# Kernel optimization log

Measured on AMD Instinct MI355X. Metric: run time of the kernel, lower is better.

Reference implementation:

```python
import jax, jax.numpy as jnp
import numpy as np

B, S, D, E, F, A = 4096, 256, 128, 64, 4, 32
CD = D * F              # combined_dim = 512
LEVEL_N = [16, 4, 1]    # aggregators per tree level (fan_in**i for i=2,1,0)
TOTAL = E + sum(LEVEL_N)  # 85 embeddings stacked

def _init(key, shape, fan_in):
    return jax.random.normal(key, shape, jnp.float32) / np.sqrt(fan_in)

def setup_inputs() -> dict:
    key = jax.random.key(0)
    ks = iter(jax.random.split(key, 64))
    inp = {"state": jax.random.normal(next(ks), (B, S), jnp.float32)}
    # 64 encoder FNNs: S -> D -> D -> D, stacked along leading node axis
    inp["enc_w1"] = _init(next(ks), (E, S, D), S); inp["enc_b1"] = jnp.zeros((E, D), jnp.float32)
    inp["enc_wh"] = _init(next(ks), (E, D, D), D); inp["enc_bh"] = jnp.zeros((E, D), jnp.float32)
    inp["enc_wo"] = _init(next(ks), (E, D, D), D); inp["enc_bo"] = jnp.zeros((E, D), jnp.float32)
    # aggregator FNNs per level: CD -> CD -> CD -> D
    for li, n in enumerate(LEVEL_N):
        inp[f"agg{li}_w1"] = _init(next(ks), (n, CD, CD), CD); inp[f"agg{li}_b1"] = jnp.zeros((n, CD), jnp.float32)
        inp[f"agg{li}_wh"] = _init(next(ks), (n, CD, CD), CD); inp[f"agg{li}_bh"] = jnp.zeros((n, CD), jnp.float32)
        inp[f"agg{li}_wo"] = _init(next(ks), (n, CD, D), CD);  inp[f"agg{li}_bo"] = jnp.zeros((n, D), jnp.float32)
    # head FNN: D -> D -> D -> A
    inp["head_w1"] = _init(next(ks), (D, D), D); inp["head_b1"] = jnp.zeros((D,), jnp.float32)
    inp["head_wh"] = _init(next(ks), (D, D), D); inp["head_bh"] = jnp.zeros((D,), jnp.float32)
    inp["head_wo"] = _init(next(ks), (D, A), D); inp["head_bo"] = jnp.zeros((A,), jnp.float32)
    return inp

def _fnn(x, w1, b1, wh, bh, wo, bo):
    # x: [N,B,I] batched over N independent same-shaped FNNs (grouped GEMM form)
    h = jax.nn.relu(jnp.einsum('nbi,nih->nbh', x, w1) + b1[:, None])
    h = jax.nn.relu(jnp.einsum('nbh,nhk->nbk', h, wh) + bh[:, None])
    return jnp.einsum('nbh,nho->nbo', h, wo) + bo[:, None]

def _forward(state, enc_w1, enc_b1, enc_wh, enc_bh, enc_wo, enc_bo,
             agg0_w1, agg0_b1, agg0_wh, agg0_bh, agg0_wo, agg0_bo,
             agg1_w1, agg1_b1, agg1_wh, agg1_bh, agg1_wo, agg1_bo,
             agg2_w1, agg2_b1, agg2_wh, agg2_bh, agg2_wo, agg2_bo,
             head_w1, head_b1, head_wh, head_bh, head_wo, head_bo):
    # encoders: state [B,S] shared across all E encoders
    h = jax.nn.relu(jnp.einsum('bs,nsh->nbh', state, enc_w1) + enc_b1[:, None])
    h = jax.nn.relu(jnp.einsum('nbh,nhk->nbk', h, enc_wh) + enc_bh[:, None])
    prev = jnp.einsum('nbh,nho->nbo', h, enc_wo) + enc_bo[:, None]   # [E,B,D]
    all_embeds = [prev]
    levels = [(agg0_w1, agg0_b1, agg0_wh, agg0_bh, agg0_wo, agg0_bo),
              (agg1_w1, agg1_b1, agg1_wh, agg1_bh, agg1_wo, agg1_bo),
              (agg2_w1, agg2_b1, agg2_wh, agg2_bh, agg2_wo, agg2_bo)]
    for (w1, b1, wh, bh, wo, bo) in levels:
        n = prev.shape[0] // F
        # concat fan-in sibling embeddings along feature dim: [n,B,F*D]
        x = prev.reshape(n, F, B, D).transpose(0, 2, 1, 3).reshape(n, B, F * D)
        prev = _fnn(x, w1, b1, wh, bh, wo, bo)                        # [n,B,D]
        all_embeds.append(prev)
    root = prev[0]                                                    # [B,D]
    hh = jax.nn.relu(root @ head_w1 + head_b1)
    hh = jax.nn.relu(hh @ head_wh + head_bh)
    action = jnp.tanh(hh @ head_wo + head_bo)                         # noise_std=0.0, action_tanh=True
    embeds = jnp.transpose(jnp.concatenate(all_embeds, axis=0), (1, 0, 2))  # [B,85,D]
    return embeds, action

def reference(state, enc_w1, enc_b1, enc_wh, enc_bh, enc_wo, enc_bo,
              agg0_w1, agg0_b1, agg0_wh, agg0_bh, agg0_wo, agg0_bo,
              agg1_w1, agg1_b1, agg1_wh, agg1_bh, agg1_wo, agg1_bo,
              agg2_w1, agg2_b1, agg2_wh, agg2_bh, agg2_wo, agg2_bo,
              head_w1, head_b1, head_wh, head_bh, head_wo, head_bo):
    return _forward(state, enc_w1, enc_b1, enc_wh, enc_bh, enc_wo, enc_bo,
                    agg0_w1, agg0_b1, agg0_wh, agg0_bh, agg0_wo, agg0_bo,
                    agg1_w1, agg1_b1, agg1_wh, agg1_bh, agg1_wo, agg1_bo,
                    agg2_w1, agg2_b1, agg2_wh, agg2_bh, agg2_wo, agg2_bo,
                    head_w1, head_b1, head_wh, head_bh, head_wo, head_bo)
```

## Files before the change

### kernel.cpp

```cpp
#include <hip/hip_runtime.h>
#include <math.h>

typedef unsigned short u16;
typedef __bf16 bf16x8 __attribute__((ext_vector_type(8)));
typedef float  f32x4  __attribute__((ext_vector_type(4)));

__device__ __forceinline__ u16 f2bf(float f) {
    unsigned int u = __float_as_uint(f);
    u = (u + 0x7FFFu + ((u >> 16) & 1u)) >> 16;
    return (u16)u;
}

__device__ __forceinline__ void gload16(const u16* g, u16* l) {
    __builtin_amdgcn_global_load_lds(
        (const __attribute__((address_space(1))) void*)g,
        (__attribute__((address_space(3))) void*)l, 16, 0, 0);
}

struct TJob { const float* src; u16* dst; int K, N, tpg, gbase, mode; };
struct TTab { TJob j[16]; };

__global__ void transpose_multi(TTab tab, int njobs) {
    __shared__ u16 tile[32][33];
    int bid = blockIdx.x;
    int ji = 0;
#pragma unroll 1
    for (int t = 1; t < njobs; ++t)
        if (bid >= tab.j[t].gbase) ji = t;
    TJob jb = tab.j[ji];
    int t = bid - jb.gbase;
    if (jb.mode == 1) {
        long off = (long)t * 1024 + threadIdx.x * 4;
        float4 x = *(const float4*)(jb.src + off);
        ushort4 o;
        o.x = f2bf(x.x); o.y = f2bf(x.y); o.z = f2bf(x.z); o.w = f2bf(x.w);
        *(ushort4*)(jb.dst + off) = o;
        return;
    }
    int g = t / jb.tpg, r = t % jb.tpg;
    int nt = jb.N >> 5;
    int k0 = (r / nt) * 32, n0 = (r % nt) * 32;
    const float* s = jb.src + (long)g * jb.K * jb.N;
    u16* d = jb.dst + (long)g * jb.K * jb.N;
    int tx = threadIdx.x & 31, ty = threadIdx.x >> 5;
#pragma unroll
    for (int rr = ty; rr < 32; rr += 8)
        tile[rr][tx] = f2bf(s[(long)(k0 + rr) * jb.N + n0 + tx]);
    __syncthreads();
#pragma unroll
    for (int rr = ty; rr < 32; rr += 8)
        d[(long)(n0 + rr) * jb.K + k0 + tx] = tile[tx][rr];
}

__global__ __launch_bounds__(256, 2)
void fnn_chain128(const u16* __restrict__ X, long sXg, int ldx, int K1,
                  const u16* __restrict__ W1t, const float* __restrict__ b1,
                  const u16* __restrict__ Wht, const float* __restrict__ bh,
                  const u16* __restrict__ Wot, const float* __restrict__ bo,
                  int Do, int act3,
                  float* __restrict__ Cf, long sCfg, int ldcf,
                  u16* __restrict__ Cb, long sCbg, int ldcb)
{
    __shared__ __align__(16) u16 As[2][128 * 32];
    __shared__ __align__(16) u16 Bs[2][128 * 32];
    __shared__ __align__(16) u16 h[128 * 152];

    const int g   = blockIdx.y;
    const int m0  = blockIdx.x * 128;
    const int tid = threadIdx.x;
    const int lane = tid & 63, wv = tid >> 6;
    const int wm = wv & 1, wn = wv >> 1;
    const int lr = lane & 15, lq = lane >> 4;
    const int row0 = tid >> 2, c8 = (tid & 3) * 8;

    const u16* a_src = X + (long)g * sXg + (long)(m0 + row0) * ldx + c8;
    const u16* w1r   = W1t + (long)g * 128 * K1 + (long)row0 * K1 + c8;
    const u16* whr   = Wht + (long)g * 128 * 128 + (long)row0 * 128 + c8;

    const f32x4 z4 = {0.f, 0.f, 0.f, 0.f};
    f32x4 acc[4][4];
#pragma unroll
    for (int i = 0; i < 4; ++i)
#pragma unroll
        for (int j = 0; j < 4; ++j) acc[i][j] = z4;

    const int KT1 = K1 >> 5;
    auto stage1 = [&](int buf, int k0) {
        gload16(a_src + k0,                  &As[buf][row0 * 32 + c8]);
        gload16(a_src + (long)64 * ldx + k0, &As[buf][(row0 + 64) * 32 + c8]);
        gload16(w1r + k0,                    &Bs[buf][row0 * 32 + c8]);
        gload16(w1r + (long)64 * K1 + k0,    &Bs[buf][(row0 + 64) * 32 + c8]);
    };
    stage1(0, 0);
    __syncthreads();
    for (int kt = 0; kt < KT1; ++kt) {
        int cur = kt & 1;
        if (kt + 1 < KT1) stage1(cur ^ 1, (kt + 1) * 32);
        bf16x8 af[4], bw[4];
#pragma unroll
        for (int i = 0; i < 4; ++i)
            af[i] = *(const bf16x8*)&As[cur][(wm * 64 + i * 16 + lr) * 32 + lq * 8];
#pragma unroll
        for (int j = 0; j < 4; ++j)
            bw[j] = *(const bf16x8*)&Bs[cur][(wn * 64 + j * 16 + lr) * 32 + lq * 8];
#pragma unroll
        for (int i = 0; i < 4; ++i)
#pragma unroll
            for (int j = 0; j < 4; ++j)
                acc[i][j] = __builtin_amdgcn_mfma_f32_16x16x32_bf16(
                    af[i], bw[j], acc[i][j], 0, 0, 0);
        __syncthreads();
    }
    {
        const float* bg = b1 + (long)g * 128;
#pragma unroll
        for (int j = 0; j < 4; ++j) {
            int n = wn * 64 + j * 16 + lr;
            float bb = bg[n];
#pragma unroll
            for (int i = 0; i < 4; ++i) {
                int mb = wm * 64 + i * 16 + lq * 4;
#pragma unroll
                for (int r = 0; r < 4; ++r)
                    h[(mb + r) * 152 + n] = f2bf(fmaxf(acc[i][j][r] + bb, 0.f));
            }
        }
    }

#pragma unroll
    for (int i = 0; i < 4; ++i)
#pragma unroll
        for (int j = 0; j < 4; ++j) acc[i][j] = z4;
    auto stage2 = [&](int buf, int k0) {
        gload16(whr + k0,                  &Bs[buf][row0 * 32 + c8]);
        gload16(whr + (long)64 * 128 + k0, &Bs[buf][(row0 + 64) * 32 + c8]);
    };
    stage2(0, 0);
    __syncthreads();
    for (int kt = 0; kt < 4; ++kt) {
        int cur = kt & 1;
        if (kt + 1 < 4) stage2(cur ^ 1, (kt + 1) * 32);
        bf16x8 af[4], bw[4];
#pragma unroll
        for (int i = 0; i < 4; ++i)
            af[i] = *(const bf16x8*)&h[(wm * 64 + i * 16 + lr) * 152 + kt * 32 + lq * 8];
#pragma unroll
        for (int j = 0; j < 4; ++j)
            bw[j] = *(const bf16x8*)&Bs[cur][(wn * 64 + j * 16 + lr) * 32 + lq * 8];
#pragma unroll
        for (int i = 0; i < 4; ++i)
#pragma unroll
            for (int j = 0; j < 4; ++j)
                acc[i][j] = __builtin_amdgcn_mfma_f32_16x16x32_bf16(
                    af[i], bw[j], acc[i][j], 0, 0, 0);
        __syncthreads();
    }
    {
        const float* bg = bh + (long)g * 128;
#pragma unroll
        for (int j = 0; j < 4; ++j) {
            int n = wn * 64 + j * 16 + lr;
            float bb = bg[n];
#pragma unroll
            for (int i = 0; i < 4; ++i) {
                int mb = wm * 64 + i * 16 + lq * 4;
#pragma unroll
                for (int r = 0; r < 4; ++r)
                    h[(mb + r) * 152 + n] = f2bf(fmaxf(acc[i][j][r] + bb, 0.f));
            }
        }
    }

#pragma unroll
    for (int i = 0; i < 4; ++i)
#pragma unroll
        for (int j = 0; j < 4; ++j) acc[i][j] = z4;
    const int nr0 = (row0 < Do) ? row0 : Do - 1;
    const int nr1 = (row0 + 64 < Do) ? row0 + 64 : Do - 1;
    const u16* wor0 = Wot + (long)g * Do * 128 + (long)nr0 * 128 + c8;
    const u16* wor1 = Wot + (long)g * Do * 128 + (long)nr1 * 128 + c8;
    auto stage3 = [&](int buf, int k0) {
        gload16(wor0 + k0, &Bs[buf][row0 * 32 + c8]);
        gload16(wor1 + k0, &Bs[buf][(row0 + 64) * 32 + c8]);
    };
    stage3(0, 0);
    __syncthreads();
    for (int kt = 0; kt < 4; ++kt) {
        int cur = kt & 1;
        if (kt + 1 < 4) stage3(cur ^ 1, (kt + 1) * 32);
        bf16x8 af[4], bw[4];
#pragma unroll
        for (int i = 0; i < 4; ++i)
            af[i] = *(const bf16x8*)&h[(wm * 64 + i * 16 + lr) * 152 + kt * 32 + lq * 8];
#pragma unroll
        for (int j = 0; j < 4; ++j)
            bw[j] = *(const bf16x8*)&Bs[cur][(wn * 64 + j * 16 + lr) * 32 + lq * 8];
#pragma unroll
        for (int i = 0; i < 4; ++i)
#pragma unroll
            for (int j = 0; j < 4; ++j)
                acc[i][j] = __builtin_amdgcn_mfma_f32_16x16x32_bf16(
                    af[i], bw[j], acc[i][j], 0, 0, 0);
        __syncthreads();
    }
    {
        const float* bg = bo + (long)g * Do;
#pragma unroll
        for (int j = 0; j < 4; ++j) {
            int n = wn * 64 + j * 16 + lr;
            if (n >= Do) continue;
            float bb = bg[n];
#pragma unroll
            for (int i = 0; i < 4; ++i) {
                int mb = wm * 64 + i * 16 + lq * 4;
#pragma unroll
                for (int r = 0; r < 4; ++r) {
                    float v = acc[i][j][r] + bb;
                    if (act3 == 2) v = tanhf(v);
                    long mrow = m0 + mb + r;
                    Cf[(long)g * sCfg + mrow * ldcf + n] = v;
                    if (Cb) Cb[(long)g * sCbg + mrow * ldcb + n] = f2bf(v);
                }
            }
        }
    }
}

__global__ __launch_bounds__(512, 2)
void fnn_chain512(const u16* __restrict__ X, long sXg, int ldx,
                  const u16* __restrict__ W1t, const float* __restrict__ b1,
                  const u16* __restrict__ Wht, const float* __restrict__ bh,
                  const u16* __restrict__ Wot, const float* __restrict__ bo,
                  float* __restrict__ Cf, long sCfg, int ldcf,
                  u16* __restrict__ Cb, long sCbg, int ldcb)
{
    __shared__ __align__(16) u16 As[2][64 * 32];
    __shared__ __align__(16) u16 Bs[2][512 * 32];
    __shared__ __align__(16) u16 h[64 * 536];

    const int g   = blockIdx.y;
    const int m0  = blockIdx.x * 64;
    const int tid = threadIdx.x;
    const int lane = tid & 63, wv = tid >> 6;
    const int lr = lane & 15, lq = lane >> 4;
    const int row0 = tid >> 2, c8 = (tid & 3) * 8;

    const u16* a_src = X + (long)g * sXg + (long)(m0 + row0) * ldx + c8;
    const u16* w1r = W1t + (long)g * 512 * 512 + (long)row0 * 512 + c8;
    const u16* whr = Wht + (long)g * 512 * 512 + (long)row0 * 512 + c8;
    const u16* wor = Wot + (long)g * 128 * 512 + (long)row0 * 512 + c8;

    const f32x4 z4 = {0.f, 0.f, 0.f, 0.f};
    f32x4 acc[4][4];
#pragma unroll
    for (int i = 0; i < 4; ++i)
#pragma unroll
        for (int j = 0; j < 4; ++j) acc[i][j] = z4;

    auto stage1 = [&](int buf, int k0) {
        if (tid < 256) gload16(a_src + k0, &As[buf][row0 * 32 + c8]);
#pragma unroll
        for (int r = 0; r < 4; ++r)
            gload16(w1r + (long)(128 * r) * 512 + k0,
                    &Bs[buf][(row0 + 128 * r) * 32 + c8]);
    };
    stage1(0, 0);
    __syncthreads();
    for (int kt = 0; kt < 16; ++kt) {
        int cur = kt & 1;
        if (kt + 1 < 16) stage1(cur ^ 1, (kt + 1) * 32);
        bf16x8 af[4], bw[4];
#pragma unroll
        for (int i = 0; i < 4; ++i)
            af[i] = *(const bf16x8*)&As[cur][(i * 16 + lr) * 32 + lq * 8];
#pragma unroll
        for (int j = 0; j < 4; ++j)
            bw[j] = *(const bf16x8*)&Bs[cur][(wv * 64 + j * 16 + lr) * 32 + lq * 8];
#pragma unroll
        for (int i = 0; i < 4; ++i)
#pragma unroll
            for (int j = 0; j < 4; ++j)
                acc[i][j] = __builtin_amdgcn_mfma_f32_16x16x32_bf16(
                    af[i], bw[j], acc[i][j], 0, 0, 0);
        __syncthreads();
    }
    {
        const float* bg = b1 + (long)g * 512;
#pragma unroll
        for (int j = 0; j < 4; ++j) {
            int n = wv * 64 + j * 16 + lr;
            float bb = bg[n];
#pragma unroll
            for (int i = 0; i < 4; ++i) {
                int mb = i * 16 + lq * 4;
#pragma unroll
                for (int r = 0; r < 4; ++r)
                    h[(mb + r) * 536 + n] = f2bf(fmaxf(acc[i][j][r] + bb, 0.f));
            }
        }
    }

#pragma unroll
    for (int i = 0; i < 4; ++i)
#pragma unroll
        for (int j = 0; j < 4; ++j) acc[i][j] = z4;
    auto stage2 = [&](int buf, int k0) {
#pragma unroll
        for (int r = 0; r < 4; ++r)
            gload16(whr + (long)(128 * r) * 512 + k0,
                    &Bs[buf][(row0 + 128 * r) * 32 + c8]);
    };
    stage2(0, 0);
    __syncthreads();
    for (int kt = 0; kt < 16; ++kt) {
        int cur = kt & 1;
        if (kt + 1 < 16) stage2(cur ^ 1, (kt + 1) * 32);
        bf16x8 af[4], bw[4];
#pragma unroll
        for (int i = 0; i < 4; ++i)
            af[i] = *(const bf16x8*)&h[(i * 16 + lr) * 536 + kt * 32 + lq * 8];
#pragma unroll
        for (int j = 0; j < 4; ++j)
            bw[j] = *(const bf16x8*)&Bs[cur][(wv * 64 + j * 16 + lr) * 32 + lq * 8];
#pragma unroll
        for (int i = 0; i < 4; ++i)
#pragma unroll
            for (int j = 0; j < 4; ++j)
                acc[i][j] = __builtin_amdgcn_mfma_f32_16x16x32_bf16(
                    af[i], bw[j], acc[i][j], 0, 0, 0);
        __syncthreads();
    }
    {
        const float* bg = bh + (long)g * 512;
#pragma unroll
        for (int j = 0; j < 4; ++j) {
            int n = wv * 64 + j * 16 + lr;
            float bb = bg[n];
#pragma unroll
            for (int i = 0; i < 4; ++i) {
                int mb = i * 16 + lq * 4;
#pragma unroll
                for (int r = 0; r < 4; ++r)
                    h[(mb + r) * 536 + n] = f2bf(fmaxf(acc[i][j][r] + bb, 0.f));
            }
        }
    }

    const int wm3 = wv & 1, wn3 = wv >> 1;
    f32x4 a2[2][2];
#pragma unroll
    for (int i = 0; i < 2; ++i)
#pragma unroll
        for (int j = 0; j < 2; ++j) a2[i][j] = z4;
    auto stage3 = [&](int buf, int k0) {
        gload16(wor + k0, &Bs[buf][row0 * 32 + c8]);
    };
    stage3(0, 0);
    __syncthreads();
    for (int kt = 0; kt < 16; ++kt) {
        int cur = kt & 1;
        if (kt + 1 < 16) stage3(cur ^ 1, (kt + 1) * 32);
        bf16x8 af2[2], bw2[2];
#pragma unroll
        for (int i = 0; i < 2; ++i)
            af2[i] = *(const bf16x8*)&h[(wm3 * 32 + i * 16 + lr) * 536 + kt * 32 + lq * 8];
#pragma unroll
        for (int j = 0; j < 2; ++j)
            bw2[j] = *(const bf16x8*)&Bs[cur][(wn3 * 32 + j * 16 + lr) * 32 + lq * 8];
#pragma unroll
        for (int i = 0; i < 2; ++i)
#pragma unroll
            for (int j = 0; j < 2; ++j)
                a2[i][j] = __builtin_amdgcn_mfma_f32_16x16x32_bf16(
                    af2[i], bw2[j], a2[i][j], 0, 0, 0);
        __syncthreads();
    }
    {
        const float* bg = bo + (long)g * 128;
#pragma unroll
        for (int j = 0; j < 2; ++j) {
            int n = wn3 * 32 + j * 16 + lr;
            float bb = bg[n];
#pragma unroll
            for (int i = 0; i < 2; ++i) {
                int mb = wm3 * 32 + i * 16 + lq * 4;
#pragma unroll
                for (int r = 0; r < 4; ++r) {
                    float v = a2[i][j][r] + bb;
                    long mrow = m0 + mb + r;
                    Cf[(long)g * sCfg + mrow * ldcf + n] = v;
                    if (Cb) Cb[(long)g * sCbg + mrow * ldcb + n] = f2bf(v);
                }
            }
        }
    }
}

extern "C" void kernel_launch(void* const* d_in, const int* in_sizes, int n_in,
                              void* d_out, int out_size, void* d_ws, size_t ws_size,
                              hipStream_t stream) {
    const int B = 4096, S = 256, D = 128, NA = 32, CD = 512;

    const float* state   = (const float*)d_in[0];
    const float* enc_w1  = (const float*)d_in[1];
    const float* enc_b1  = (const float*)d_in[2];
    const float* enc_wh  = (const float*)d_in[3];
    const float* enc_bh  = (const float*)d_in[4];
    const float* enc_wo  = (const float*)d_in[5];
    const float* enc_bo  = (const float*)d_in[6];
    const float *agg_w1[3], *agg_b1[3], *agg_wh[3], *agg_bh[3], *agg_wo[3], *agg_bo[3];
    for (int l = 0; l < 3; ++l) {
        agg_w1[l] = (const float*)d_in[7 + 6 * l + 0];
        agg_b1[l] = (const float*)d_in[7 + 6 * l + 1];
        agg_wh[l] = (const float*)d_in[7 + 6 * l + 2];
        agg_bh[l] = (const float*)d_in[7 + 6 * l + 3];
        agg_wo[l] = (const float*)d_in[7 + 6 * l + 4];
        agg_bo[l] = (const float*)d_in[7 + 6 * l + 5];
    }
    const float* head_w1 = (const float*)d_in[25];
    const float* head_b1 = (const float*)d_in[26];
    const float* head_wh = (const float*)d_in[27];
    const float* head_bh = (const float*)d_in[28];
    const float* head_wo = (const float*)d_in[29];
    const float* head_bo = (const float*)d_in[30];

    float* out    = (float*)d_out;
    float* action = out + (long)B * 85 * D;

    char* wsp = (char*)d_ws;
    auto carve = [&](long elems) {
        u16* p = (u16*)wsp;
        wsp += ((elems * 2 + 255) / 256) * 256;
        return p;
    };
    u16* enc_w1t = carve(64L * 128 * 256);
    u16* enc_wht = carve(64L * 128 * 128);
    u16* enc_wot = carve(64L * 128 * 128);
    u16 *agg_w1t[3], *agg_wht[3], *agg_wot[3];
    const int LN[3] = {16, 4, 1};
    for (int l = 0; l < 3; ++l) {
        agg_w1t[l] = carve((long)LN[l] * 512 * 512);
        agg_wht[l] = carve((long)LN[l] * 512 * 512);
        agg_wot[l] = carve((long)LN[l] * 128 * 512);
    }
    u16* head_w1t = carve(128L * 128);
    u16* head_wht = carve(128L * 128);
    u16* head_wot = carve(32L * 128);
    u16* stateB = carve((long)B * S);
    u16* bufA   = carve(33554432L);
    u16* bufB   = carve(33554432L);

    TTab tab = {};
    int nj = 0, base = 0;
    auto addT = [&](const float* s, u16* d, int G, int K, int N) {
        int tpg = (K / 32) * (N / 32);
        tab.j[nj] = {s, d, K, N, tpg, base, 0};
        base += G * tpg; ++nj;
    };
    auto addC = [&](const float* s, u16* d, long elems) {
        tab.j[nj] = {s, d, 0, 0, 0, base, 1};
        base += (int)(elems / 1024); ++nj;
    };
    addT(enc_w1, enc_w1t, 64, 256, 128);
    addT(enc_wh, enc_wht, 64, 128, 128);
    addT(enc_wo, enc_wot, 64, 128, 128);
    for (int l = 0; l < 3; ++l) {
        addT(agg_w1[l], agg_w1t[l], LN[l], 512, 512);
        addT(agg_wh[l], agg_wht[l], LN[l], 512, 512);
        addT(agg_wo[l], agg_wot[l], LN[l], 512, 128);
    }
    addT(head_w1, head_w1t, 1, 128, 128);
    addT(head_wh, head_wht, 1, 128, 128);
    addT(head_wo, head_wot, 1, 128, 32);
    addC(state, stateB, (long)B * S);
    transpose_multi<<<base, 256, 0, stream>>>(tab, nj);

    const int LD = 85 * D;

    fnn_chain128<<<dim3(32, 64), 256, 0, stream>>>(
        stateB, 0, S, 256,
        enc_w1t, enc_b1, enc_wht, enc_bh, enc_wot, enc_bo, 128, 0,
        out, D, LD, bufA, D, 64 * D);

    fnn_chain512<<<dim3(64, 16), 512, 0, stream>>>(
        bufA, 512, 64 * D,
        agg_w1t[0], agg_b1[0], agg_wht[0], agg_bh[0], agg_wot[0], agg_bo[0],
        out + 64L * D, D, LD, bufB, D, 16 * D);

    fnn_chain512<<<dim3(64, 4), 512, 0, stream>>>(
        bufB, 512, 16 * D,
        agg_w1t[1], agg_b1[1], agg_wht[1], agg_bh[1], agg_wot[1], agg_bo[1],
        out + 80L * D, D, LD, bufA, D, 4 * D);

    fnn_chain512<<<dim3(64, 1), 512, 0, stream>>>(
        bufA, 0, 4 * D,
        agg_w1t[2], agg_b1[2], agg_wht[2], agg_bh[2], agg_wot[2], agg_bo[2],
        out + 84L * D, D, LD, bufB, 0, D);

    fnn_chain128<<<dim3(32, 1), 256, 0, stream>>>(
        bufB, 0, D, 128,
        head_w1t, head_b1, head_wht, head_bh, head_wot, head_bo, 32, 2,
        action, 0, NA, nullptr, 0, 0);
}
```

Baseline: 702.0 us.

## Halve row tiles, XOR-swizzle hidden LDS buffer, and split aggregator N into passes

Both fused FNN chain kernels now process half as many batch rows per block: 64 for the encoder/head kernel and 32 for the aggregator kernel. The aggregator kernel drops from 512 to 256 threads and computes its 512-wide hidden layers in two 256-column passes. The hidden activation buffer replaces padding with an XOR swizzle, which shrinks LDS and avoids bank conflicts. The aim is more blocks and higher occupancy, especially for the small last tree levels, at the cost of loading each weight tile twice as often per batch row.

```diff
diff --git a/kernel.cpp b/kernel.cpp
--- a/kernel.cpp
+++ b/kernel.cpp
@@ -15,6 +15,10 @@
     __builtin_amdgcn_global_load_lds(
         (const __attribute__((address_space(1))) void*)g,
         (__attribute__((address_space(3))) void*)l, 16, 0, 0);
+}
+
+__device__ __forceinline__ int hswz(int row, int col, int ld) {
+    return (row * ld + col) ^ ((row & 7) << 3);
 }
 
 struct TJob { const float* src; u16* dst; int K, N, tpg, gbase, mode; };
@@ -52,7 +56,7 @@
         d[(long)(n0 + rr) * jb.K + k0 + tx] = tile[tx][rr];
 }
 
-__global__ __launch_bounds__(256, 2)
+__global__ __launch_bounds__(256, 4)
 void fnn_chain128(const u16* __restrict__ X, long sXg, int ldx, int K1,
                   const u16* __restrict__ W1t, const float* __restrict__ b1,
                   const u16* __restrict__ Wht, const float* __restrict__ bh,
@@ -61,50 +65,49 @@
                   float* __restrict__ Cf, long sCfg, int ldcf,
                   u16* __restrict__ Cb, long sCbg, int ldcb)
 {
-    __shared__ __align__(16) u16 As[2][128 * 32];
+    __shared__ __align__(16) u16 As[2][64 * 32];
     __shared__ __align__(16) u16 Bs[2][128 * 32];
-    __shared__ __align__(16) u16 h[128 * 152];
+    __shared__ __align__(16) u16 h[64 * 128];
 
     const int g   = blockIdx.y;
-    const int m0  = blockIdx.x * 128;
+    const int m0  = blockIdx.x * 64;
     const int tid = threadIdx.x;
     const int lane = tid & 63, wv = tid >> 6;
     const int wm = wv & 1, wn = wv >> 1;
     const int lr = lane & 15, lq = lane >> 4;
-    const int row0 = tid >> 2, c8 = (tid & 3) * 8;
-
-    const u16* a_src = X + (long)g * sXg + (long)(m0 + row0) * ldx + c8;
-    const u16* w1r   = W1t + (long)g * 128 * K1 + (long)row0 * K1 + c8;
-    const u16* whr   = Wht + (long)g * 128 * 128 + (long)row0 * 128 + c8;
+    const int arow = tid >> 2, akc = (tid & 3) * 8;
+
+    const u16* a_src = X + (long)g * sXg + (long)(m0 + arow) * ldx + akc;
+    const u16* w1r   = W1t + (long)g * 128 * K1 + (long)arow * K1 + akc;
+    const u16* whr   = Wht + (long)g * 128 * 128 + (long)arow * 128 + akc;
 
     const f32x4 z4 = {0.f, 0.f, 0.f, 0.f};
-    f32x4 acc[4][4];
-#pragma unroll
-    for (int i = 0; i < 4; ++i)
+    f32x4 acc[2][4];
+#pragma unroll
+    for (int i = 0; i < 2; ++i)
 #pragma unroll
         for (int j = 0; j < 4; ++j) acc[i][j] = z4;
 
     const int KT1 = K1 >> 5;
     auto stage1 = [&](int buf, int k0) {
-        gload16(a_src + k0,                  &As[buf][row0 * 32 + c8]);
-        gload16(a_src + (long)64 * ldx + k0, &As[buf][(row0 + 64) * 32 + c8]);
-        gload16(w1r + k0,                    &Bs[buf][row0 * 32 + c8]);
-        gload16(w1r + (long)64 * K1 + k0,    &Bs[buf][(row0 + 64) * 32 + c8]);
+        gload16(a_src + k0, &As[buf][arow * 32 + akc]);
+        gload16(w1r + k0,                   &Bs[buf][arow * 32 + akc]);
+        gload16(w1r + (long)64 * K1 + k0,   &Bs[buf][(arow + 64) * 32 + akc]);
     };
     stage1(0, 0);
     __syncthreads();
     for (int kt = 0; kt < KT1; ++kt) {
         int cur = kt & 1;
         if (kt + 1 < KT1) stage1(cur ^ 1, (kt + 1) * 32);
-        bf16x8 af[4], bw[4];
-#pragma unroll
-        for (int i = 0; i < 4; ++i)
-            af[i] = *(const bf16x8*)&As[cur][(wm * 64 + i * 16 + lr) * 32 + lq * 8];
+        bf16x8 af[2], bw[4];
+#pragma unroll
+        for (int i = 0; i < 2; ++i)
+            af[i] = *(const bf16x8*)&As[cur][(wm * 32 + i * 16 + lr) * 32 + lq * 8];
 #pragma unroll
         for (int j = 0; j < 4; ++j)
             bw[j] = *(const bf16x8*)&Bs[cur][(wn * 64 + j * 16 + lr) * 32 + lq * 8];
 #pragma unroll
-        for (int i = 0; i < 4; ++i)
+        for (int i = 0; i < 2; ++i)
 #pragma unroll
             for (int j = 0; j < 4; ++j)
                 acc[i][j] = __builtin_amdgcn_mfma_f32_16x16x32_bf16(
@@ -118,37 +121,39 @@
             int n = wn * 64 + j * 16 + lr;
             float bb = bg[n];
 #pragma unroll
-            for (int i = 0; i < 4; ++i) {
-                int mb = wm * 64 + i * 16 + lq * 4;
+            for (int i = 0; i < 2; ++i) {
+                int mb = wm * 32 + i * 16 + lq * 4;
 #pragma unroll
                 for (int r = 0; r < 4; ++r)
-                    h[(mb + r) * 152 + n] = f2bf(fmaxf(acc[i][j][r] + bb, 0.f));
-            }
-        }
-    }
-
-#pragma unroll
-    for (int i = 0; i < 4; ++i)
+                    h[hswz(mb + r, n, 128)] = f2bf(fmaxf(acc[i][j][r] + bb, 0.f));
+            }
+        }
+    }
+
+#pragma unroll
+    for (int i = 0; i < 2; ++i)
 #pragma unroll
         for (int j = 0; j < 4; ++j) acc[i][j] = z4;
     auto stage2 = [&](int buf, int k0) {
-        gload16(whr + k0,                  &Bs[buf][row0 * 32 + c8]);
-        gload16(whr + (long)64 * 128 + k0, &Bs[buf][(row0 + 64) * 32 + c8]);
+        gload16(whr + k0,                  &Bs[buf][arow * 32 + akc]);
+        gload16(whr + (long)64 * 128 + k0, &Bs[buf][(arow + 64) * 32 + akc]);
     };
     stage2(0, 0);
     __syncthreads();
     for (int kt = 0; kt < 4; ++kt) {
         int cur = kt & 1;
         if (kt + 1 < 4) stage2(cur ^ 1, (kt + 1) * 32);
-        bf16x8 af[4], bw[4];
-#pragma unroll
-        for (int i = 0; i < 4; ++i)
-            af[i] = *(const bf16x8*)&h[(wm * 64 + i * 16 + lr) * 152 + kt * 32 + lq * 8];
+        bf16x8 af[2], bw[4];
+#pragma unroll
+        for (int i = 0; i < 2; ++i) {
+            int row = wm * 32 + i * 16 + lr;
+            af[i] = *(const bf16x8*)&h[hswz(row, kt * 32 + lq * 8, 128)];
+        }
 #pragma unroll
         for (int j = 0; j < 4; ++j)
             bw[j] = *(const bf16x8*)&Bs[cur][(wn * 64 + j * 16 + lr) * 32 + lq * 8];
 #pragma unroll
-        for (int i = 0; i < 4; ++i)
+        for (int i = 0; i < 2; ++i)
 #pragma unroll
             for (int j = 0; j < 4; ++j)
                 acc[i][j] = __builtin_amdgcn_mfma_f32_16x16x32_bf16(
@@ -162,41 +167,43 @@
             int n = wn * 64 + j * 16 + lr;
             float bb = bg[n];
 #pragma unroll
-            for (int i = 0; i < 4; ++i) {
-                int mb = wm * 64 + i * 16 + lq * 4;
+            for (int i = 0; i < 2; ++i) {
+                int mb = wm * 32 + i * 16 + lq * 4;
 #pragma unroll
                 for (int r = 0; r < 4; ++r)
-                    h[(mb + r) * 152 + n] = f2bf(fmaxf(acc[i][j][r] + bb, 0.f));
-            }
-        }
-    }
-
-#pragma unroll
-    for (int i = 0; i < 4; ++i)
+                    h[hswz(mb + r, n, 128)] = f2bf(fmaxf(acc[i][j][r] + bb, 0.f));
+            }
+        }
+    }
+
+#pragma unroll
+    for (int i = 0; i < 2; ++i)
 #pragma unroll
         for (int j = 0; j < 4; ++j) acc[i][j] = z4;
-    const int nr0 = (row0 < Do) ? row0 : Do - 1;
-    const int nr1 = (row0 + 64 < Do) ? row0 + 64 : Do - 1;
-    const u16* wor0 = Wot + (long)g * Do * 128 + (long)nr0 * 128 + c8;
-    const u16* wor1 = Wot + (long)g * Do * 128 + (long)nr1 * 128 + c8;
+    const int nr0 = (arow < Do) ? arow : Do - 1;
+    const int nr1 = (arow + 64 < Do) ? arow + 64 : Do - 1;
+    const u16* wor0 = Wot + (long)g * Do * 128 + (long)nr0 * 128 + akc;
+    const u16* wor1 = Wot + (long)g * Do * 128 + (long)nr1 * 128 + akc;
     auto stage3 = [&](int buf, int k0) {
-        gload16(wor0 + k0, &Bs[buf][row0 * 32 + c8]);
-        gload16(wor1 + k0, &Bs[buf][(row0 + 64) * 32 + c8]);
+        gload16(wor0 + k0, &Bs[buf][arow * 32 + akc]);
+        gload16(wor1 + k0, &Bs[buf][(arow + 64) * 32 + akc]);
     };
     stage3(0, 0);
     __syncthreads();
     for (int kt = 0; kt < 4; ++kt) {
         int cur = kt & 1;
         if (kt + 1 < 4) stage3(cur ^ 1, (kt + 1) * 32);
-        bf16x8 af[4], bw[4];
-#pragma unroll
-        for (int i = 0; i < 4; ++i)
-            af[i] = *(const bf16x8*)&h[(wm * 64 + i * 16 + lr) * 152 + kt * 32 + lq * 8];
+        bf16x8 af[2], bw[4];
+#pragma unroll
+        for (int i = 0; i < 2; ++i) {
+            int row = wm * 32 + i * 16 + lr;
+            af[i] = *(const bf16x8*)&h[hswz(row, kt * 32 + lq * 8, 128)];
+        }
 #pragma unroll
         for (int j = 0; j < 4; ++j)
             bw[j] = *(const bf16x8*)&Bs[cur][(wn * 64 + j * 16 + lr) * 32 + lq * 8];
 #pragma unroll
-        for (int i = 0; i < 4; ++i)
+        for (int i = 0; i < 2; ++i)
 #pragma unroll
             for (int j = 0; j < 4; ++j)
                 acc[i][j] = __builtin_amdgcn_mfma_f32_16x16x32_bf16(
@@ -211,8 +218,8 @@
             if (n >= Do) continue;
             float bb = bg[n];
 #pragma unroll
-            for (int i = 0; i < 4; ++i) {
-                int mb = wm * 64 + i * 16 + lq * 4;
+            for (int i = 0; i < 2; ++i) {
+                int mb = wm * 32 + i * 16 + lq * 4;
 #pragma unroll
                 for (int r = 0; r < 4; ++r) {
                     float v = acc[i][j][r] + bb;
@@ -226,7 +233,7 @@
     }
 }
 
-__global__ __launch_bounds__(512, 2)
+__global__ __launch_bounds__(256, 2)
 void fnn_chain512(const u16* __restrict__ X, long sXg, int ldx,
                   const u16* __restrict__ W1t, const float* __restrict__ b1,
                   const u16* __restrict__ Wht, const float* __restrict__ bh,
@@ -234,159 +241,178 @@
                   float* __restrict__ Cf, long sCfg, int ldcf,
                   u16* __restrict__ Cb, long sCbg, int ldcb)
 {
-    __shared__ __align__(16) u16 As[2][64 * 32];
-    __shared__ __align__(16) u16 Bs[2][512 * 32];
-    __shared__ __align__(16) u16 h[64 * 536];
+    __shared__ __align__(16) u16 As[2][32 * 32];
+    __shared__ __align__(16) u16 Bs[2][256 * 32];
+    __shared__ __align__(16) u16 h[32 * 512];
 
     const int g   = blockIdx.y;
-    const int m0  = blockIdx.x * 64;
+    const int m0  = blockIdx.x * 32;
     const int tid = threadIdx.x;
     const int lane = tid & 63, wv = tid >> 6;
     const int lr = lane & 15, lq = lane >> 4;
-    const int row0 = tid >> 2, c8 = (tid & 3) * 8;
-
-    const u16* a_src = X + (long)g * sXg + (long)(m0 + row0) * ldx + c8;
-    const u16* w1r = W1t + (long)g * 512 * 512 + (long)row0 * 512 + c8;
-    const u16* whr = Wht + (long)g * 512 * 512 + (long)row0 * 512 + c8;
-    const u16* wor = Wot + (long)g * 128 * 512 + (long)row0 * 512 + c8;
+    const int arow = tid >> 2, akc = (tid & 3) * 8;
+
+    const u16* w1g = W1t + (long)g * 512 * 512;
+    const u16* whg = Wht + (long)g * 512 * 512;
+    const u16* wog = Wot + (long)g * 128 * 512;
 
     const f32x4 z4 = {0.f, 0.f, 0.f, 0.f};
-    f32x4 acc[4][4];
-#pragma unroll
-    for (int i = 0; i < 4; ++i)
-#pragma unroll
-        for (int j = 0; j < 4; ++j) acc[i][j] = z4;
-
-    auto stage1 = [&](int buf, int k0) {
-        if (tid < 256) gload16(a_src + k0, &As[buf][row0 * 32 + c8]);
+
+    auto stageL1 = [&](int buf, int p, int k0) {
+        if (tid < 128)
+            gload16(X + (long)g * sXg + (long)(m0 + arow) * ldx + akc + k0,
+                    &As[buf][arow * 32 + akc]);
+        const u16* wb = w1g + (long)(p * 256 + arow) * 512 + akc + k0;
 #pragma unroll
         for (int r = 0; r < 4; ++r)
-            gload16(w1r + (long)(128 * r) * 512 + k0,
-                    &Bs[buf][(row0 + 128 * r) * 32 + c8]);
-    };
-    stage1(0, 0);
+            gload16(wb + (long)(64 * r) * 512, &Bs[buf][(r * 64 + arow) * 32 + akc]);
+    };
+    for (int p = 0; p < 2; ++p) {
+        f32x4 acc[2][4];
+#pragma unroll
+        for (int i = 0; i < 2; ++i)
+#pragma unroll
+            for (int j = 0; j < 4; ++j) acc[i][j] = z4;
+        stageL1(0, p, 0);
+        __syncthreads();
+        for (int kt = 0; kt < 16; ++kt) {
+            int cur = kt & 1;
+            if (kt + 1 < 16) stageL1(cur ^ 1, p, (kt + 1) * 32);
+            bf16x8 af[2], bw[4];
+#pragma unroll
+            for (int i = 0; i < 2; ++i)
+                af[i] = *(const bf16x8*)&As[cur][(i * 16 + lr) * 32 + lq * 8];
+#pragma unroll
+            for (int j = 0; j < 4; ++j)
+                bw[j] = *(const bf16x8*)&Bs[cur][(wv * 64 + j * 16 + lr) * 32 + lq * 8];
+#pragma unroll
+            for (int i = 0; i < 2; ++i)
+#pragma unroll
+                for (int j = 0; j < 4; ++j)
+                    acc[i][j] = __builtin_amdgcn_mfma_f32_16x16x32_bf16(
+                        af[i], bw[j], acc[i][j], 0, 0, 0);
+            __syncthreads();
+        }
+        const float* bg = b1 + (long)g * 512 + p * 256;
+#pragma unroll
+        for (int j = 0; j < 4; ++j) {
+            int nl = wv * 64 + j * 16 + lr;
+            float bb = bg[nl];
+#pragma unroll
+            for (int i = 0; i < 2; ++i) {
+                int mb = i * 16 + lq * 4;
+#pragma unroll
+                for (int r = 0; r < 4; ++r)
+                    h[hswz(mb + r, p * 256 + nl, 512)] =
+                        f2bf(fmaxf(acc[i][j][r] + bb, 0.f));
+            }
+        }
+    }
+
+    f32x4 acc2[2][2][4];
+#pragma unroll
+    for (int p = 0; p < 2; ++p)
+#pragma unroll
+        for (int i = 0; i < 2; ++i)
+#pragma unroll
+            for (int j = 0; j < 4; ++j) acc2[p][i][j] = z4;
+    auto stageL2 = [&](int buf, int p, int k0) {
+        const u16* wb = whg + (long)(p * 256 + arow) * 512 + akc + k0;
+#pragma unroll
+        for (int r = 0; r < 4; ++r)
+            gload16(wb + (long)(64 * r) * 512, &Bs[buf][(r * 64 + arow) * 32 + akc]);
+    };
+    stageL2(0, 0, 0);
+    __syncthreads();
+#pragma unroll
+    for (int p = 0; p < 2; ++p) {
+#pragma unroll 1
+        for (int kt = 0; kt < 16; ++kt) {
+            const int s = p * 16 + kt;
+            const int cur = s & 1;
+            if (s + 1 < 32) stageL2(cur ^ 1, (s + 1) >> 4, ((s + 1) & 15) * 32);
+            bf16x8 af[2], bw[4];
+#pragma unroll
+            for (int i = 0; i < 2; ++i) {
+                int row = i * 16 + lr;
+                af[i] = *(const bf16x8*)&h[hswz(row, kt * 32 + lq * 8, 512)];
+            }
+#pragma unroll
+            for (int j = 0; j < 4; ++j)
+                bw[j] = *(const bf16x8*)&Bs[cur][(wv * 64 + j * 16 + lr) * 32 + lq * 8];
+#pragma unroll
+            for (int i = 0; i < 2; ++i)
+#pragma unroll
+                for (int j = 0; j < 4; ++j)
+                    acc2[p][i][j] = __builtin_amdgcn_mfma_f32_16x16x32_bf16(
+                        af[i], bw[j], acc2[p][i][j], 0, 0, 0);
+            __syncthreads();
+        }
+    }
+    {
+        const float* bg = bh + (long)g * 512;
+#pragma unroll
+        for (int p = 0; p < 2; ++p)
+#pragma unroll
+            for (int j = 0; j < 4; ++j) {
+                int nl = wv * 64 + j * 16 + lr;
+                float bb = bg[p * 256 + nl];
+#pragma unroll
+                for (int i = 0; i < 2; ++i) {
+                    int mb = i * 16 + lq * 4;
+#pragma unroll
+                    for (int r = 0; r < 4; ++r)
+                        h[hswz(mb + r, p * 256 + nl, 512)] =
+                            f2bf(fmaxf(acc2[p][i][j][r] + bb, 0.f));
+                }
+            }
+    }
+
+    f32x4 acc3[2][2];
+#pragma unroll
+    for (int i = 0; i < 2; ++i)
+#pragma unroll
+        for (int j = 0; j < 2; ++j) acc3[i][j] = z4;
+    auto stageL3 = [&](int buf, int k0) {
+        const u16* wb = wog + (long)arow * 512 + akc + k0;
+#pragma unroll
+        for (int r = 0; r < 2; ++r)
+            gload16(wb + (long)(64 * r) * 512, &Bs[buf][(r * 64 + arow) * 32 + akc]);
+    };
+    stageL3(0, 0);
     __syncthreads();
     for (int kt = 0; kt < 16; ++kt) {
         int cur = kt & 1;
-        if (kt + 1 < 16) stage1(cur ^ 1, (kt + 1) * 32);
-        bf16x8 af[4], bw[4];
-#pragma unroll
-        for (int i = 0; i < 4; ++i)
-            af[i] = *(const bf16x8*)&As[cur][(i * 16 + lr) * 32 + lq * 8];
-#pragma unroll
-        for (int j = 0; j < 4; ++j)
-            bw[j] = *(const bf16x8*)&Bs[cur][(wv * 64 + j * 16 + lr) * 32 + lq * 8];
-#pragma unroll
-        for (int i = 0; i < 4; ++i)
-#pragma unroll
-            for (int j = 0; j < 4; ++j)
-                acc[i][j] = __builtin_amdgcn_mfma_f32_16x16x32_bf16(
-                    af[i], bw[j], acc[i][j], 0, 0, 0);
-        __syncthreads();
-    }
-    {
-        const float* bg = b1 + (long)g * 512;
-#pragma unroll
-        for (int j = 0; j < 4; ++j) {
-            int n = wv * 64 + j * 16 + lr;
-            float bb = bg[n];
-#pragma unroll
-            for (int i = 0; i < 4; ++i) {
-                int mb = i * 16 + lq * 4;
-#pragma unroll
-                for (int r = 0; r < 4; ++r)
-                    h[(mb + r) * 536 + n] = f2bf(fmaxf(acc[i][j][r] + bb, 0.f));
-            }
-        }
-    }
-
-#pragma unroll
-    for (int i = 0; i < 4; ++i)
-#pragma unroll
-        for (int j = 0; j < 4; ++j) acc[i][j] = z4;
-    auto stage2 = [&](int buf, int k0) {
-#pragma unroll
-        for (int r = 0; r < 4; ++r)
-            gload16(whr + (long)(128 * r) * 512 + k0,
-                    &Bs[buf][(row0 + 128 * r) * 32 + c8]);
-    };
-    stage2(0, 0);
-    __syncthreads();
-    for (int kt = 0; kt < 16; ++kt) {
-        int cur = kt & 1;
-        if (kt + 1 < 16) stage2(cur ^ 1, (kt + 1) * 32);
-        bf16x8 af[4], bw[4];
-#pragma unroll
-        for (int i = 0; i < 4; ++i)
-            af[i] = *(const bf16x8*)&h[(i * 16 + lr) * 536 + kt * 32 + lq * 8];
-#pragma unroll
-        for (int j = 0; j < 4; ++j)
-            bw[j] = *(const bf16x8*)&Bs[cur][(wv * 64 + j * 16 + lr) * 32 + lq * 8];
-#pragma unroll
-        for (int i = 0; i < 4; ++i)
-#pragma unroll
-            for (int j = 0; j < 4; ++j)
-                acc[i][j] = __builtin_amdgcn_mfma_f32_16x16x32_bf16(
-                    af[i], bw[j], acc[i][j], 0, 0, 0);
-        __syncthreads();
-    }
-    {
-        const float* bg = bh + (long)g * 512;
-#pragma unroll
-        for (int j = 0; j < 4; ++j) {
-            int n = wv * 64 + j * 16 + lr;
-            float bb = bg[n];
-#pragma unroll
-            for (int i = 0; i < 4; ++i) {
-                int mb = i * 16 + lq * 4;
-#pragma unroll
-                for (int r = 0; r < 4; ++r)
-                    h[(mb + r) * 536 + n] = f2bf(fmaxf(acc[i][j][r] + bb, 0.f));
-            }
-        }
-    }
-
-    const int wm3 = wv & 1, wn3 = wv >> 1;
-    f32x4 a2[2][2];
-#pragma unroll
-    for (int i = 0; i < 2; ++i)
-#pragma unroll
-        for (int j = 0; j < 2; ++j) a2[i][j] = z4;
-    auto stage3 = [&](int buf, int k0) {
-        gload16(wor + k0, &Bs[buf][row0 * 32 + c8]);
-    };
-    stage3(0, 0);
-    __syncthreads();
-    for (int kt = 0; kt < 16; ++kt) {
-        int cur = kt & 1;
-        if (kt + 1 < 16) stage3(cur ^ 1, (kt + 1) * 32);
-        bf16x8 af2[2], bw2[2];
-#pragma unroll
-        for (int i = 0; i < 2; ++i)
-            af2[i] = *(const bf16x8*)&h[(wm3 * 32 + i * 16 + lr) * 536 + kt * 32 + lq * 8];
+        if (kt + 1 < 16) stageL3(cur ^ 1, (kt + 1) * 32);
+        bf16x8 af[2], bw[2];
+#pragma unroll
+        for (int i = 0; i < 2; ++i) {
+            int row = i * 16 + lr;
+            af[i] = *(const bf16x8*)&h[hswz(row, kt * 32 + lq * 8, 512)];
+        }
 #pragma unroll
         for (int j = 0; j < 2; ++j)
-            bw2[j] = *(const bf16x8*)&Bs[cur][(wn3 * 32 + j * 16 + lr) * 32 + lq * 8];
+            bw[j] = *(const bf16x8*)&Bs[cur][(wv * 32 + j * 16 + lr) * 32 + lq * 8];
 #pragma unroll
         for (int i = 0; i < 2; ++i)
 #pragma unroll
             for (int j = 0; j < 2; ++j)
-                a2[i][j] = __builtin_amdgcn_mfma_f32_16x16x32_bf16(
-                    af2[i], bw2[j], a2[i][j], 0, 0, 0);
+                acc3[i][j] = __builtin_amdgcn_mfma_f32_16x16x32_bf16(
+                    af[i], bw[j], acc3[i][j], 0, 0, 0);
         __syncthreads();
     }
     {
         const float* bg = bo + (long)g * 128;
 #pragma unroll
         for (int j = 0; j < 2; ++j) {
-            int n = wn3 * 32 + j * 16 + lr;
+            int n = wv * 32 + j * 16 + lr;
             float bb = bg[n];
 #pragma unroll
             for (int i = 0; i < 2; ++i) {
-                int mb = wm3 * 32 + i * 16 + lq * 4;
+                int mb = i * 16 + lq * 4;
 #pragma unroll
                 for (int r = 0; r < 4; ++r) {
-                    float v = a2[i][j][r] + bb;
+                    float v = acc3[i][j][r] + bb;
                     long mrow = m0 + mb + r;
                     Cf[(long)g * sCfg + mrow * ldcf + n] = v;
                     if (Cb) Cb[(long)g * sCbg + mrow * ldcb + n] = f2bf(v);
@@ -477,27 +503,27 @@
 
     const int LD = 85 * D;
 
-    fnn_chain128<<<dim3(32, 64), 256, 0, stream>>>(
+    fnn_chain128<<<dim3(64, 64), 256, 0, stream>>>(
         stateB, 0, S, 256,
         enc_w1t, enc_b1, enc_wht, enc_bh, enc_wot, enc_bo, 128, 0,
         out, D, LD, bufA, D, 64 * D);
 
-    fnn_chain512<<<dim3(64, 16), 512, 0, stream>>>(
+    fnn_chain512<<<dim3(128, 16), 256, 0, stream>>>(
         bufA, 512, 64 * D,
         agg_w1t[0], agg_b1[0], agg_wht[0], agg_bh[0], agg_wot[0], agg_bo[0],
         out + 64L * D, D, LD, bufB, D, 16 * D);
 
-    fnn_chain512<<<dim3(64, 4), 512, 0, stream>>>(
+    fnn_chain512<<<dim3(128, 4), 256, 0, stream>>>(
         bufB, 512, 16 * D,
         agg_w1t[1], agg_b1[1], agg_wht[1], agg_bh[1], agg_wot[1], agg_bo[1],
         out + 80L * D, D, LD, bufA, D, 4 * D);
 
-    fnn_chain512<<<dim3(64, 1), 512, 0, stream>>>(
+    fnn_chain512<<<dim3(128, 1), 256, 0, stream>>>(
         bufA, 0, 4 * D,
         agg_w1t[2], agg_b1[2], agg_wht[2], agg_bh[2], agg_wot[2], agg_bo[2],
         out + 84L * D, D, LD, bufB, 0, D);
 
-    fnn_chain128<<<dim3(32, 1), 256, 0, stream>>>(
+    fnn_chain128<<<dim3(64, 1), 256, 0, stream>>>(
         bufB, 0, D, 128,
         head_w1t, head_b1, head_wht, head_bh, head_wot, head_bo, 32, 2,
         action, 0, NA, nullptr, 0, 0);
```

After: 752.2 us. +7.1%, slower.

## Shrink encoder tile to 64 rows, swizzle LDS hidden buffer, XCD-aware block mapping

Applied to the files above, without the earlier changes.

The 128-input FNN chain kernel now uses 64-row M tiles with a 128-column hidden buffer addressed through an XOR swizzle instead of padding. This cuts LDS use and lets launch bounds request 4 blocks per CU. All chain kernels switch to a 1D grid whose block index is decoded so that blocks sharing the same weight group land on the same XCD, aiming for better L2 reuse of weights. Smaller tiles mean B weights are re-read from L2 twice as often per output row.

```diff
diff --git a/kernel.cpp b/kernel.cpp
--- a/kernel.cpp
+++ b/kernel.cpp
@@ -15,6 +15,23 @@
     __builtin_amdgcn_global_load_lds(
         (const __attribute__((address_space(1))) void*)g,
         (__attribute__((address_space(3))) void*)l, 16, 0, 0);
+}
+
+__device__ __forceinline__ int hswz(int row, int col, int ld) {
+    return (row * ld + col) ^ ((row & 7) << 3);
+}
+
+__device__ __forceinline__ void xcd_decode(int bid, int n_g, int& mb, int& g) {
+    int xcd = bid & 7, j = bid >> 3;
+    if (n_g >= 8) {
+        int gpx = n_g >> 3;
+        g  = xcd * gpx + (j % gpx);
+        mb = j / gpx;
+    } else {
+        int xpg = 8 / n_g;
+        g  = xcd / xpg;
+        mb = j * xpg + (xcd % xpg);
+    }
 }
 
 struct TJob { const float* src; u16* dst; int K, N, tpg, gbase, mode; };
@@ -52,8 +69,9 @@
         d[(long)(n0 + rr) * jb.K + k0 + tx] = tile[tx][rr];
 }
 
-__global__ __launch_bounds__(256, 2)
-void fnn_chain128(const u16* __restrict__ X, long sXg, int ldx, int K1,
+__global__ __launch_bounds__(256, 4)
+void fnn_chain128(int n_g,
+                  const u16* __restrict__ X, long sXg, int ldx, int K1,
                   const u16* __restrict__ W1t, const float* __restrict__ b1,
                   const u16* __restrict__ Wht, const float* __restrict__ bh,
                   const u16* __restrict__ Wot, const float* __restrict__ bo,
@@ -61,50 +79,50 @@
                   float* __restrict__ Cf, long sCfg, int ldcf,
                   u16* __restrict__ Cb, long sCbg, int ldcb)
 {
-    __shared__ __align__(16) u16 As[2][128 * 32];
+    __shared__ __align__(16) u16 As[2][64 * 32];
     __shared__ __align__(16) u16 Bs[2][128 * 32];
-    __shared__ __align__(16) u16 h[128 * 152];
-
-    const int g   = blockIdx.y;
-    const int m0  = blockIdx.x * 128;
+    __shared__ __align__(16) u16 h[64 * 128];
+
+    int mb, g;
+    xcd_decode(blockIdx.x, n_g, mb, g);
+    const int m0  = mb * 64;
     const int tid = threadIdx.x;
     const int lane = tid & 63, wv = tid >> 6;
     const int wm = wv & 1, wn = wv >> 1;
     const int lr = lane & 15, lq = lane >> 4;
-    const int row0 = tid >> 2, c8 = (tid & 3) * 8;
-
-    const u16* a_src = X + (long)g * sXg + (long)(m0 + row0) * ldx + c8;
-    const u16* w1r   = W1t + (long)g * 128 * K1 + (long)row0 * K1 + c8;
-    const u16* whr   = Wht + (long)g * 128 * 128 + (long)row0 * 128 + c8;
+    const int arow = tid >> 2, akc = (tid & 3) * 8;
+
+    const u16* a_src = X + (long)g * sXg + (long)(m0 + arow) * ldx + akc;
+    const u16* w1r   = W1t + (long)g * 128 * K1 + (long)arow * K1 + akc;
+    const u16* whr   = Wht + (long)g * 128 * 128 + (long)arow * 128 + akc;
 
     const f32x4 z4 = {0.f, 0.f, 0.f, 0.f};
-    f32x4 acc[4][4];
-#pragma unroll
-    for (int i = 0; i < 4; ++i)
+    f32x4 acc[2][4];
+#pragma unroll
+    for (int i = 0; i < 2; ++i)
 #pragma unroll
         for (int j = 0; j < 4; ++j) acc[i][j] = z4;
 
     const int KT1 = K1 >> 5;
     auto stage1 = [&](int buf, int k0) {
-        gload16(a_src + k0,                  &As[buf][row0 * 32 + c8]);
-        gload16(a_src + (long)64 * ldx + k0, &As[buf][(row0 + 64) * 32 + c8]);
-        gload16(w1r + k0,                    &Bs[buf][row0 * 32 + c8]);
-        gload16(w1r + (long)64 * K1 + k0,    &Bs[buf][(row0 + 64) * 32 + c8]);
+        gload16(a_src + k0, &As[buf][arow * 32 + akc]);
+        gload16(w1r + k0,                   &Bs[buf][arow * 32 + akc]);
+        gload16(w1r + (long)64 * K1 + k0,   &Bs[buf][(arow + 64) * 32 + akc]);
     };
     stage1(0, 0);
     __syncthreads();
     for (int kt = 0; kt < KT1; ++kt) {
         int cur = kt & 1;
         if (kt + 1 < KT1) stage1(cur ^ 1, (kt + 1) * 32);
-        bf16x8 af[4], bw[4];
-#pragma unroll
-        for (int i = 0; i < 4; ++i)
-            af[i] = *(const bf16x8*)&As[cur][(wm * 64 + i * 16 + lr) * 32 + lq * 8];
+        bf16x8 af[2], bw[4];
+#pragma unroll
+        for (int i = 0; i < 2; ++i)
+            af[i] = *(const bf16x8*)&As[cur][(wm * 32 + i * 16 + lr) * 32 + lq * 8];
 #pragma unroll
         for (int j = 0; j < 4; ++j)
             bw[j] = *(const bf16x8*)&Bs[cur][(wn * 64 + j * 16 + lr) * 32 + lq * 8];
 #pragma unroll
-        for (int i = 0; i < 4; ++i)
+        for (int i = 0; i < 2; ++i)
 #pragma unroll
             for (int j = 0; j < 4; ++j)
                 acc[i][j] = __builtin_amdgcn_mfma_f32_16x16x32_bf16(
@@ -118,37 +136,39 @@
             int n = wn * 64 + j * 16 + lr;
             float bb = bg[n];
 #pragma unroll
-            for (int i = 0; i < 4; ++i) {
-                int mb = wm * 64 + i * 16 + lq * 4;
+            for (int i = 0; i < 2; ++i) {
+                int mb2 = wm * 32 + i * 16 + lq * 4;
 #pragma unroll
                 for (int r = 0; r < 4; ++r)
-                    h[(mb + r) * 152 + n] = f2bf(fmaxf(acc[i][j][r] + bb, 0.f));
+                    h[hswz(mb2 + r, n, 128)] = f2bf(fmaxf(acc[i][j][r] + bb, 0.f));
             }
         }
     }
 
 #pragma unroll
-    for (int i = 0; i < 4; ++i)
+    for (int i = 0; i < 2; ++i)
 #pragma unroll
         for (int j = 0; j < 4; ++j) acc[i][j] = z4;
     auto stage2 = [&](int buf, int k0) {
-        gload16(whr + k0,                  &Bs[buf][row0 * 32 + c8]);
-        gload16(whr + (long)64 * 128 + k0, &Bs[buf][(row0 + 64) * 32 + c8]);
+        gload16(whr + k0,                  &Bs[buf][arow * 32 + akc]);
+        gload16(whr + (long)64 * 128 + k0, &Bs[buf][(arow + 64) * 32 + akc]);
     };
     stage2(0, 0);
     __syncthreads();
     for (int kt = 0; kt < 4; ++kt) {
         int cur = kt & 1;
         if (kt + 1 < 4) stage2(cur ^ 1, (kt + 1) * 32);
-        bf16x8 af[4], bw[4];
-#pragma unroll
-        for (int i = 0; i < 4; ++i)
-            af[i] = *(const bf16x8*)&h[(wm * 64 + i * 16 + lr) * 152 + kt * 32 + lq * 8];
+        bf16x8 af[2], bw[4];
+#pragma unroll
+        for (int i = 0; i < 2; ++i) {
+            int row = wm * 32 + i * 16 + lr;
+            af[i] = *(const bf16x8*)&h[hswz(row, kt * 32 + lq * 8, 128)];
+        }
 #pragma unroll
         for (int j = 0; j < 4; ++j)
             bw[j] = *(const bf16x8*)&Bs[cur][(wn * 64 + j * 16 + lr) * 32 + lq * 8];
 #pragma unroll
-        for (int i = 0; i < 4; ++i)
+        for (int i = 0; i < 2; ++i)
 #pragma unroll
             for (int j = 0; j < 4; ++j)
                 acc[i][j] = __builtin_amdgcn_mfma_f32_16x16x32_bf16(
@@ -162,41 +182,43 @@
             int n = wn * 64 + j * 16 + lr;
             float bb = bg[n];
 #pragma unroll
-            for (int i = 0; i < 4; ++i) {
-                int mb = wm * 64 + i * 16 + lq * 4;
+            for (int i = 0; i < 2; ++i) {
+                int mb2 = wm * 32 + i * 16 + lq * 4;
 #pragma unroll
                 for (int r = 0; r < 4; ++r)
-                    h[(mb + r) * 152 + n] = f2bf(fmaxf(acc[i][j][r] + bb, 0.f));
+                    h[hswz(mb2 + r, n, 128)] = f2bf(fmaxf(acc[i][j][r] + bb, 0.f));
             }
         }
     }
 
 #pragma unroll
-    for (int i = 0; i < 4; ++i)
+    for (int i = 0; i < 2; ++i)
 #pragma unroll
         for (int j = 0; j < 4; ++j) acc[i][j] = z4;
-    const int nr0 = (row0 < Do) ? row0 : Do - 1;
-    const int nr1 = (row0 + 64 < Do) ? row0 + 64 : Do - 1;
-    const u16* wor0 = Wot + (long)g * Do * 128 + (long)nr0 * 128 + c8;
-    const u16* wor1 = Wot + (long)g * Do * 128 + (long)nr1 * 128 + c8;
+    const int nr0 = (arow < Do) ? arow : Do - 1;
+    const int nr1 = (arow + 64 < Do) ? arow + 64 : Do - 1;
+    const u16* wor0 = Wot + (long)g * Do * 128 + (long)nr0 * 128 + akc;
+    const u16* wor1 = Wot + (long)g * Do * 128 + (long)nr1 * 128 + akc;
     auto stage3 = [&](int buf, int k0) {
-        gload16(wor0 + k0, &Bs[buf][row0 * 32 + c8]);
-        gload16(wor1 + k0, &Bs[buf][(row0 + 64) * 32 + c8]);
+        gload16(wor0 + k0, &Bs[buf][arow * 32 + akc]);
+        gload16(wor1 + k0, &Bs[buf][(arow + 64) * 32 + akc]);
     };
     stage3(0, 0);
     __syncthreads();
     for (int kt = 0; kt < 4; ++kt) {
         int cur = kt & 1;
         if (kt + 1 < 4) stage3(cur ^ 1, (kt + 1) * 32);
-        bf16x8 af[4], bw[4];
-#pragma unroll
-        for (int i = 0; i < 4; ++i)
-            af[i] = *(const bf16x8*)&h[(wm * 64 + i * 16 + lr) * 152 + kt * 32 + lq * 8];
+        bf16x8 af[2], bw[4];
+#pragma unroll
+        for (int i = 0; i < 2; ++i) {
+            int row = wm * 32 + i * 16 + lr;
+            af[i] = *(const bf16x8*)&h[hswz(row, kt * 32 + lq * 8, 128)];
+        }
 #pragma unroll
         for (int j = 0; j < 4; ++j)
             bw[j] = *(const bf16x8*)&Bs[cur][(wn * 64 + j * 16 + lr) * 32 + lq * 8];
 #pragma unroll
-        for (int i = 0; i < 4; ++i)
+        for (int i = 0; i < 2; ++i)
 #pragma unroll
             for (int j = 0; j < 4; ++j)
                 acc[i][j] = __builtin_amdgcn_mfma_f32_16x16x32_bf16(
@@ -211,13 +233,13 @@
             if (n >= Do) continue;
             float bb = bg[n];
 #pragma unroll
-            for (int i = 0; i < 4; ++i) {
-                int mb = wm * 64 + i * 16 + lq * 4;
+            for (int i = 0; i < 2; ++i) {
+                int mb2 = wm * 32 + i * 16 + lq * 4;
 #pragma unroll
                 for (int r = 0; r < 4; ++r) {
                     float v = acc[i][j][r] + bb;
                     if (act3 == 2) v = tanhf(v);
-                    long mrow = m0 + mb + r;
+                    long mrow = m0 + mb2 + r;
                     Cf[(long)g * sCfg + mrow * ldcf + n] = v;
                     if (Cb) Cb[(long)g * sCbg + mrow * ldcb + n] = f2bf(v);
                 }
@@ -227,7 +249,8 @@
 }
 
 __global__ __launch_bounds__(512, 2)
-void fnn_chain512(const u16* __restrict__ X, long sXg, int ldx,
+void fnn_chain512(int n_g,
+                  const u16* __restrict__ X, long sXg, int ldx,
                   const u16* __restrict__ W1t, const float* __restrict__ b1,
                   const u16* __restrict__ Wht, const float* __restrict__ bh,
                   const u16* __restrict__ Wot, const float* __restrict__ bo,
@@ -238,8 +261,9 @@
     __shared__ __align__(16) u16 Bs[2][512 * 32];
     __shared__ __align__(16) u16 h[64 * 536];
 
-    const int g   = blockIdx.y;
-    const int m0  = blockIdx.x * 64;
+    int mb, g;
+    xcd_decode(blockIdx.x, n_g, mb, g);
+    const int m0  = mb * 64;
     const int tid = threadIdx.x;
     const int lane = tid & 63, wv = tid >> 6;
     const int lr = lane & 15, lq = lane >> 4;
@@ -292,10 +316,10 @@
             float bb = bg[n];
 #pragma unroll
             for (int i = 0; i < 4; ++i) {
-                int mb = i * 16 + lq * 4;
+                int mb2 = i * 16 + lq * 4;
 #pragma unroll
                 for (int r = 0; r < 4; ++r)
-                    h[(mb + r) * 536 + n] = f2bf(fmaxf(acc[i][j][r] + bb, 0.f));
+                    h[(mb2 + r) * 536 + n] = f2bf(fmaxf(acc[i][j][r] + bb, 0.f));
             }
         }
     }
@@ -338,10 +362,10 @@
             float bb = bg[n];
 #pragma unroll
             for (int i = 0; i < 4; ++i) {
-                int mb = i * 16 + lq * 4;
+                int mb2 = i * 16 + lq * 4;
 #pragma unroll
                 for (int r = 0; r < 4; ++r)
-                    h[(mb + r) * 536 + n] = f2bf(fmaxf(acc[i][j][r] + bb, 0.f));
+                    h[(mb2 + r) * 536 + n] = f2bf(fmaxf(acc[i][j][r] + bb, 0.f));
             }
         }
     }
@@ -383,11 +407,11 @@
             float bb = bg[n];
 #pragma unroll
             for (int i = 0; i < 2; ++i) {
-                int mb = wm3 * 32 + i * 16 + lq * 4;
+                int mb2 = wm3 * 32 + i * 16 + lq * 4;
 #pragma unroll
                 for (int r = 0; r < 4; ++r) {
                     float v = a2[i][j][r] + bb;
-                    long mrow = m0 + mb + r;
+                    long mrow = m0 + mb2 + r;
                     Cf[(long)g * sCfg + mrow * ldcf + n] = v;
                     if (Cb) Cb[(long)g * sCbg + mrow * ldcb + n] = f2bf(v);
                 }
@@ -476,29 +500,30 @@
     transpose_multi<<<base, 256, 0, stream>>>(tab, nj);
 
     const int LD = 85 * D;
-
-    fnn_chain128<<<dim3(32, 64), 256, 0, stream>>>(
-        stateB, 0, S, 256,
+    const int MB64 = B / 64;
+
+    fnn_chain128<<<MB64 * 64, 256, 0, stream>>>(
+        64, stateB, 0, S, 256,
         enc_w1t, enc_b1, enc_wht, enc_bh, enc_wot, enc_bo, 128, 0,
         out, D, LD, bufA, D, 64 * D);
 
-    fnn_chain512<<<dim3(64, 16), 512, 0, stream>>>(
-        bufA, 512, 64 * D,
+    fnn_chain512<<<MB64 * 16, 512, 0, stream>>>(
+        16, bufA, 512, 64 * D,
         agg_w1t[0], agg_b1[0], agg_wht[0], agg_bh[0], agg_wot[0], agg_bo[0],
         out + 64L * D, D, LD, bufB, D, 16 * D);
 
-    fnn_chain512<<<dim3(64, 4), 512, 0, stream>>>(
-        bufB, 512, 16 * D,
+    fnn_chain512<<<MB64 * 4, 512, 0, stream>>>(
+        4, bufB, 512, 16 * D,
         agg_w1t[1], agg_b1[1], agg_wht[1], agg_bh[1], agg_wot[1], agg_bo[1],
         out + 80L * D, D, LD, bufA, D, 4 * D);
 
-    fnn_chain512<<<dim3(64, 1), 512, 0, stream>>>(
-        bufA, 0, 4 * D,
+    fnn_chain512<<<MB64, 512, 0, stream>>>(
+        1, bufA, 0, 4 * D,
         agg_w1t[2], agg_b1[2], agg_wht[2], agg_bh[2], agg_wot[2], agg_bo[2],
         out + 84L * D, D, LD, bufB, 0, D);
 
-    fnn_chain128<<<dim3(32, 1), 256, 0, stream>>>(
-        bufB, 0, D, 128,
+    fnn_chain128<<<MB64, 256, 0, stream>>>(
+        1, bufB, 0, D, 128,
         head_w1t, head_b1, head_wht, head_bh, head_wot, head_bo, 32, 2,
         action, 0, NA, nullptr, 0, 0);
 }
```

After: 648.2 us. 1.08x faster.
